# Optimization experiments

Hardware: AMD Instinct MI355X
Metric: run time of the kernel (lower is better)

The kernel has to match this reference:

```python
import jax, jax.numpy as jnp
import numpy as np

B, T, N = 16, 12, 1024
DIM_IN, DOUT, CHEB_K, EMB = 1, 64, 2, 10
TOD, DOW = 48, 7
DIN = DIM_IN + 2 * EMB  # 21: input feature + tod emb + dow emb


def _mk(key, shape, scale=0.1):
    return scale * jax.random.normal(key, shape, dtype=jnp.float32)


def setup_inputs() -> dict:
    key = jax.random.key(0)
    ks = jax.random.split(key, 16)
    data = jax.random.normal(ks[0], (B, T, N, DIM_IN), jnp.float32)
    tod = jax.random.randint(ks[1], (B, T, N), 0, TOD).astype(jnp.float32)
    dow = jax.random.randint(ks[2], (B, T, N), 0, DOW).astype(jnp.float32)
    x = jnp.concatenate([data, tod[..., None], dow[..., None]], axis=-1)
    return dict(
        x=x,
        init_state=jnp.zeros((1, B, N, DOUT), jnp.float32),
        ne_tod=jax.random.normal(ks[3], (B, T, EMB), jnp.float32),
        ne_dow=jax.random.normal(ks[4], (B, T, EMB), jnp.float32),
        node_emb=jax.random.normal(ks[5], (N, EMB), jnp.float32),
        Wtod=_mk(ks[6], (TOD, EMB)), btod=jnp.zeros((EMB,), jnp.float32),
        Wdow=_mk(ks[7], (DOW, EMB)), bdow=jnp.zeros((EMB,), jnp.float32),
        WQ=_mk(ks[8], (DOUT, DOUT)), bQ=jnp.zeros((DOUT,), jnp.float32),
        WK=_mk(ks[9], (DOUT, DOUT)), bK=jnp.zeros((DOUT,), jnp.float32),
        WV=_mk(ks[10], (DOUT, DOUT)), bV=jnp.zeros((DOUT,), jnp.float32),
        Wpool_g=_mk(ks[11], (EMB, CHEB_K, DIN + DOUT, 2 * DOUT)),
        bpool_g=_mk(ks[12], (EMB, 2 * DOUT)),
        Wpool_c=_mk(ks[13], (EMB, CHEB_K, DIN + DOUT, DOUT)),
        bpool_c=_mk(ks[14], (EMB, DOUT)),
    )


def _cheb(A, x):
    # Chebyshev basis: T0=x, T1=A@x, Tk=2A T_{k-1}-T_{k-2}. A:[B,N,N], x:[B,N,F] -> [B,K,N,F]
    outs = [x, jnp.einsum('bnm,bmf->bnf', A, x)]
    for _ in range(CHEB_K - 2):
        outs.append(2.0 * jnp.einsum('bnm,bmf->bnf', A, outs[-1]) - outs[-2])
    return jnp.stack(outs[:CHEB_K], axis=1)


def _gconv(A, x, W, b):
    # node-adaptive graph conv: W:[N,K,F,O] (per-node weights from pool), b:[N,O]
    return jnp.einsum('bknf,nkfo->bno', _cheb(A, x), W) + b


def reference(x, init_state, ne_tod, ne_dow, node_emb, Wtod, btod, Wdow, bdow,
              WQ, bQ, WK, bK, WV, bV, Wpool_g, bpool_g, Wpool_c, bpool_c):
    tod = x[..., -2].astype(jnp.int32)
    dow = x[..., -1].astype(jnp.int32)
    # one_hot @ Linear == embedding gather (same math)
    cur = jnp.concatenate([x[..., :DIM_IN], Wtod[tod] + btod, Wdow[dow] + bdow], axis=-1)

    E = node_emb
    # per-node weights/bias from pools (static over time -> hoisted out of scan)
    Wg = jnp.einsum('nd,dkfo->nkfo', E, Wpool_g)
    bg = E @ bpool_g
    Wc = jnp.einsum('nd,dkfo->nkfo', E, Wpool_c)
    bc = E @ bpool_c

    def step(h, inputs):
        x_t, e1, e2 = inputs
        # dynamic adjacency from time-modulated node embeddings
        d1 = E[None] * e1[:, None, :]  # B,N,d
        d2 = E[None] * e2[:, None, :]
        A = jax.nn.softmax(jax.nn.relu(jnp.einsum('bnd,bmd->bnm', d1, d2)), axis=-1)
        zr = jax.nn.sigmoid(_gconv(A, jnp.concatenate([x_t, h], -1), Wg, bg))
        z, r = jnp.split(zr, 2, axis=-1)
        hc = jnp.tanh(_gconv(A, jnp.concatenate([x_t, z * h], -1), Wc, bc))
        h_new = r * h + (1.0 - r) * hc
        return h_new, h_new

    xs = (jnp.moveaxis(cur, 1, 0), jnp.moveaxis(ne_tod, 1, 0), jnp.moveaxis(ne_dow, 1, 0))
    h_last, states = jax.lax.scan(step, init_state[0], xs)
    seq = jnp.moveaxis(states, 0, 1)  # B,T,N,DOUT

    # temporal self-attention (per node, over T)
    xr = jnp.swapaxes(seq, 1, 2)  # B,N,T,DOUT
    Q = xr @ WQ + bQ
    K = xr @ WK + bK
    V = xr @ WV + bV
    attn = jax.nn.softmax(jnp.einsum('bntd,bnsd->bnts', Q, K) / (DOUT ** 0.5), axis=-1)
    Z = jnp.einsum('bnts,bnsd->bntd', attn, V)
    out = jnp.swapaxes(Z, 1, 2)  # B,T,N,DOUT
    return out, h_last
```

## Files before the change

kernel.cpp:

```cpp
#include <hip/hip_runtime.h>

#define BB 16
#define TT 12
#define NN 1024
#define EMB 10
#define DIN 21
#define DOUT 64
#define FF 85
#define FP 96
#define KFP 176
#define BTN (BB * TT * NN)
#define ASCALE 256.0f
#define INV_ASCALE (1.0f / 256.0f)
#define LSCALE 4096.0f
#define INV_LSCALE (1.0f / 4096.0f)

typedef float4 f4;
typedef _Float16 f16;
typedef __attribute__((ext_vector_type(8))) _Float16 f16x8;
typedef __attribute__((ext_vector_type(4))) float f32x4;

__global__ __launch_bounds__(256) void k_embedT(const float* __restrict__ x,
    const float* __restrict__ Wtod, const float* __restrict__ btod,
    const float* __restrict__ Wdow, const float* __restrict__ bdow,
    f16* __restrict__ curh, f16* __restrict__ curl) {
  int idx = blockIdx.x * 256 + threadIdx.x;
  if (idx >= BB * TT * DIN * NN) return;
  int n = idx & 1023;
  int f = (idx >> 10) % DIN;
  int bt = idx / (DIN * 1024);
  const float* xp = x + ((size_t)bt * 1024 + n) * 3;
  float v;
  if (f == 0) v = xp[0];
  else if (f < 1 + EMB) {
    int tod = (int)xp[1];
    v = Wtod[tod * EMB + f - 1] + btod[f - 1];
  } else {
    int dow = (int)xp[2];
    v = Wdow[dow * EMB + f - 1 - EMB] + bdow[f - 1 - EMB];
  }
  f16 hi = (f16)v;
  curh[idx] = hi;
  curl[idx] = (f16)((v - (float)hi) * LSCALE);
}

__global__ __launch_bounds__(256) void k_wpT(const float* __restrict__ Wpool,
    float* __restrict__ Wp2, int O, int total) {
  int idx = blockIdx.x * 256 + threadIdx.x;
  if (idx >= total) return;
  int j = idx & 7;
  int d = (idx >> 3) % EMB;
  int kc = (idx / (8 * EMB)) % 22;
  int o = idx / (8 * EMB * 22);
  int kf = kc * 8 + j;
  Wp2[idx] = (kf < 2 * FF) ? Wpool[((size_t)d * 2 * FF + kf) * O + o] : 0.f;
}

__global__ __launch_bounds__(256) void k_poolT(const float* __restrict__ E,
    const float* __restrict__ Wp2, f16* __restrict__ Wh, f16* __restrict__ Wl,
    int O, int CH) {
  int n0 = blockIdx.y * 16;
  int c = blockIdx.x * 256 + threadIdx.x;
  __shared__ float Es[16][EMB];
  if (threadIdx.x < 16 * EMB)
    Es[threadIdx.x / EMB][threadIdx.x % EMB] =
        E[(n0 + threadIdx.x / EMB) * EMB + threadIdx.x % EMB];
  __syncthreads();
  if (c >= CH) return;
  const float* wb = Wp2 + (size_t)c * 80;
  float wv[80];
#pragma unroll
  for (int i = 0; i < 20; i++) *(f4*)&wv[i * 4] = *(const f4*)(wb + i * 4);
  for (int ni = 0; ni < 16; ni++) {
    f16x8 hv, lv;
#pragma unroll
    for (int j = 0; j < 8; j++) {
      float v = 0.f;
#pragma unroll
      for (int d = 0; d < EMB; d++) v = fmaf(Es[ni][d], wv[d * 8 + j], v);
      f16 hi = (f16)v;
      hv[j] = hi;
      lv[j] = (f16)((v - (float)hi) * LSCALE);
    }
    size_t base = ((size_t)(n0 + ni) * O * 22 + c) * 8;
    *(f16x8*)(Wh + base) = hv;
    *(f16x8*)(Wl + base) = lv;
  }
}

__global__ __launch_bounds__(256) void k_poolb(const float* __restrict__ E,
    const float* __restrict__ bpool, float* __restrict__ bvec, int O) {
  int idx = blockIdx.x * 256 + threadIdx.x;
  if (idx >= NN * O) return;
  int o = idx % O, n = idx / O;
  float a = 0.f;
#pragma unroll
  for (int d = 0; d < EMB; d++) a += E[n * EMB + d] * bpool[d * O + o];
  bvec[idx] = a;
}

__global__ __launch_bounds__(256) void k_inith(const float* __restrict__ s,
    float* __restrict__ hb, f16* __restrict__ hTh, f16* __restrict__ hTl) {
  int i = blockIdx.x * 256 + threadIdx.x;
  if (i >= BB * NN * DOUT) return;
  float v = s[i];
  hb[i] = v;
  int b = i >> 16;
  int n = (i >> 6) & 1023;
  int o = i & 63;
  f16 hi = (f16)v;
  size_t ti = (((size_t)(b * 64 + o)) << 10) + n;
  hTh[ti] = hi;
  hTl[ti] = (f16)((v - (float)hi) * LSCALE);
}

__global__ __launch_bounds__(256) void k_cvtw(const float* __restrict__ WQ,
    const float* __restrict__ WK, const float* __restrict__ WV,
    const float* __restrict__ bQ, const float* __restrict__ bK, const float* __restrict__ bV,
    f16* __restrict__ wbt, float* __restrict__ biasb) {
  int idx = blockIdx.x * 256 + threadIdx.x;
  if (idx < 3 * DOUT * DOUT) {
    int mat = idx >> 12;
    int d = (idx >> 6) & 63;
    int k = idx & 63;
    const float* W = mat == 0 ? WQ : (mat == 1 ? WK : WV);
    wbt[idx] = (f16)(W[k * DOUT + d]);
  } else if (idx < 3 * DOUT * DOUT + 192) {
    int j = idx - 3 * DOUT * DOUT;
    const float* bb = (j >> 6) == 0 ? bQ : ((j >> 6) == 1 ? bK : bV);
    biasb[j] = bb[j & 63];
  }
}

__global__ __launch_bounds__(256) void k_scores(const float* __restrict__ E,
    const float* __restrict__ ne1, const float* __restrict__ ne2, int t,
    f16* __restrict__ Ah, f16* __restrict__ Al,
    float* __restrict__ T1g, float* __restrict__ T1c) {
  int b = blockIdx.y;
  int i0 = blockIdx.x * 4;
  int tid = threadIdx.x;
  int lane = tid & 63;
  int wid = tid >> 6;
  {
    int gid = (blockIdx.y * gridDim.x + blockIdx.x) * 256 + tid;
    for (int i = gid; i < BB * NN * FP; i += 1048576) T1g[i] = 0.f;
    T1c[gid] = 0.f;
  }
  __shared__ float redm[4][4];
  __shared__ float reds[4][4];
  float g[EMB];
#pragma unroll
  for (int d = 0; d < EMB; d++)
    g[d] = ne1[(b * TT + t) * EMB + d] * ne2[(b * TT + t) * EMB + d];
  float c[4][EMB];
#pragma unroll
  for (int ii = 0; ii < 4; ii++)
#pragma unroll
    for (int d = 0; d < EMB; d++)
      c[ii][d] = E[(i0 + ii) * EMB + d] * g[d];
  float s[4][4];
#pragma unroll
  for (int jj = 0; jj < 4; jj++) {
    int j = jj * 256 + tid;
    float Ej[EMB];
#pragma unroll
    for (int d = 0; d < EMB; d++) Ej[d] = E[j * EMB + d];
#pragma unroll
    for (int ii = 0; ii < 4; ii++) {
      float acc = 0.f;
#pragma unroll
      for (int d = 0; d < EMB; d++) acc = fmaf(c[ii][d], Ej[d], acc);
      s[ii][jj] = fmaxf(acc, 0.f);
    }
  }
  float m4[4];
#pragma unroll
  for (int ii = 0; ii < 4; ii++) {
    float v = fmaxf(fmaxf(s[ii][0], s[ii][1]), fmaxf(s[ii][2], s[ii][3]));
#pragma unroll
    for (int off = 32; off > 0; off >>= 1) v = fmaxf(v, __shfl_xor(v, off));
    if (lane == 0) redm[wid][ii] = v;
  }
  __syncthreads();
#pragma unroll
  for (int ii = 0; ii < 4; ii++)
    m4[ii] = fmaxf(fmaxf(redm[0][ii], redm[1][ii]), fmaxf(redm[2][ii], redm[3][ii]));
  float e[4][4];
  float inv[4];
#pragma unroll
  for (int ii = 0; ii < 4; ii++) {
    float lsum = 0.f;
#pragma unroll
    for (int jj = 0; jj < 4; jj++) { e[ii][jj] = __expf(s[ii][jj] - m4[ii]); lsum += e[ii][jj]; }
#pragma unroll
    for (int off = 32; off > 0; off >>= 1) lsum += __shfl_xor(lsum, off);
    if (lane == 0) reds[wid][ii] = lsum;
  }
  __syncthreads();
#pragma unroll
  for (int ii = 0; ii < 4; ii++)
    inv[ii] = ASCALE / (reds[0][ii] + reds[1][ii] + reds[2][ii] + reds[3][ii]);
#pragma unroll
  for (int ii = 0; ii < 4; ii++) {
    size_t base = ((size_t)(b * NN) + i0 + ii) * NN;
#pragma unroll
    for (int jj = 0; jj < 4; jj++) {
      float a = e[ii][jj] * inv[ii];
      f16 hi = (f16)a;
      Ah[base + jj * 256 + tid] = hi;
      Al[base + jj * 256 + tid] = (f16)((a - (float)hi) * LSCALE);
    }
  }
}

__global__ __launch_bounds__(256) void k_spmv_g(
    const f16* __restrict__ Ah, const f16* __restrict__ Al,
    const f16* __restrict__ curh, const f16* __restrict__ curl, int t,
    const f16* __restrict__ hTh, const f16* __restrict__ hTl,
    float* __restrict__ Y) {
  int b = blockIdx.y;
  int i0 = blockIdx.x * 32;
  int kh = blockIdx.z;
  int tid = threadIdx.x;
  int lane = tid & 63, w = tid >> 6;
  int rg = w & 1, cg = w >> 1;
  int quad = lane >> 4, m = lane & 15;
  __shared__ __align__(16) f16 As_h[32][72];
  __shared__ __align__(16) f16 As_l[32][72];
  __shared__ __align__(16) f16 Xh[96][72];
  __shared__ __align__(16) f16 Xl[96][72];
  for (int q = tid; q < 11 * 72; q += 256) {
    int f = 85 + q / 72, j = q % 72;
    Xh[f][j] = (f16)0.f;
    Xl[f][j] = (f16)0.f;
  }
  f32x4 accH[3], accL[3];
#pragma unroll
  for (int q = 0; q < 3; q++) {
    accH[q] = (f32x4){0.f, 0.f, 0.f, 0.f};
    accL[q] = (f32x4){0.f, 0.f, 0.f, 0.f};
  }
  const f16* Ahb = Ah + ((size_t)(b * NN + i0)) * NN;
  const f16* Alb = Al + ((size_t)(b * NN + i0)) * NN;
  const f16* curhb = curh + ((size_t)(b * TT + t) * DIN) * NN;
  const f16* curlb = curl + ((size_t)(b * TT + t) * DIN) * NN;
  const f16* hThb = hTh + ((size_t)b << 16);
  const f16* hTlb = hTl + ((size_t)b << 16);
  int ar = tid >> 3, ac = (tid & 7) << 3;
  for (int j0 = kh * 512; j0 < kh * 512 + 512; j0 += 64) {
    *(int4*)&As_h[ar][ac] = *(const int4*)(Ahb + (size_t)ar * NN + j0 + ac);
    *(int4*)&As_l[ar][ac] = *(const int4*)(Alb + (size_t)ar * NN + j0 + ac);
#pragma unroll
    for (int p = 0; p < 6; p++) {
      int ch = p * 256 + tid;
      int isl = ch >= 768 ? 1 : 0;
      int idx = ch - isl * 768;
      int row = idx >> 3, cc = (idx & 7) << 3;
      if (row < 85) {
        const f16* s = row < 21
            ? ((isl ? curlb : curhb) + ((size_t)row << 10) + j0 + cc)
            : ((isl ? hTlb : hThb) + ((size_t)(row - 21) << 10) + j0 + cc);
        f16* d = (isl ? &Xl[0][0] : &Xh[0][0]) + row * 72 + cc;
        *(int4*)d = *(const int4*)s;
      }
    }
    __syncthreads();
#pragma unroll
    for (int ks = 0; ks < 2; ks++) {
      int k0 = ks * 32 + quad * 8;
      f16x8 a_h = *(const f16x8*)&As_h[rg * 16 + m][k0];
      f16x8 a_l = *(const f16x8*)&As_l[rg * 16 + m][k0];
#pragma unroll
      for (int nfi = 0; nfi < 3; nfi++) {
        int nf = cg * 3 + nfi;
        f16x8 x_h = *(const f16x8*)&Xh[nf * 16 + m][k0];
        f16x8 x_l = *(const f16x8*)&Xl[nf * 16 + m][k0];
        accH[nfi] = __builtin_amdgcn_mfma_f32_16x16x32_f16(a_h, x_h, accH[nfi], 0, 0, 0);
        accL[nfi] = __builtin_amdgcn_mfma_f32_16x16x32_f16(a_h, x_l, accL[nfi], 0, 0, 0);
        accL[nfi] = __builtin_amdgcn_mfma_f32_16x16x32_f16(a_l, x_h, accL[nfi], 0, 0, 0);
      }
    }
    __syncthreads();
  }
#pragma unroll
  for (int nfi = 0; nfi < 3; nfi++) {
    int nf = cg * 3 + nfi;
#pragma unroll
    for (int reg = 0; reg < 4; reg++) {
      int row = i0 + rg * 16 + quad * 4 + reg;
      atomicAdd(&Y[((size_t)(b * NN) + row) * FP + nf * 16 + m],
                (accH[nfi][reg] + accL[nfi][reg] * INV_LSCALE) * INV_ASCALE);
    }
  }
}

__global__ __launch_bounds__(256) void k_spmv_c(
    const f16* __restrict__ Ah, const f16* __restrict__ Al,
    const f16* __restrict__ zhTh, const f16* __restrict__ zhTl,
    float* __restrict__ Y) {
  int b = blockIdx.y;
  int i0 = blockIdx.x * 32;
  int kh = blockIdx.z;
  int tid = threadIdx.x;
  int lane = tid & 63, w = tid >> 6;
  int rg = w & 1, cg = w >> 1;
  int quad = lane >> 4, m = lane & 15;
  __shared__ __align__(16) f16 As_h[32][72];
  __shared__ __align__(16) f16 As_l[32][72];
  __shared__ __align__(16) f16 Xh[64][72];
  __shared__ __align__(16) f16 Xl[64][72];
  f32x4 accH[2], accL[2];
#pragma unroll
  for (int q = 0; q < 2; q++) {
    accH[q] = (f32x4){0.f, 0.f, 0.f, 0.f};
    accL[q] = (f32x4){0.f, 0.f, 0.f, 0.f};
  }
  const f16* Ahb = Ah + ((size_t)(b * NN + i0)) * NN;
  const f16* Alb = Al + ((size_t)(b * NN + i0)) * NN;
  const f16* zThb = zhTh + ((size_t)b << 16);
  const f16* zTlb = zhTl + ((size_t)b << 16);
  int ar = tid >> 3, ac = (tid & 7) << 3;
  for (int j0 = kh * 512; j0 < kh * 512 + 512; j0 += 64) {
    *(int4*)&As_h[ar][ac] = *(const int4*)(Ahb + (size_t)ar * NN + j0 + ac);
    *(int4*)&As_l[ar][ac] = *(const int4*)(Alb + (size_t)ar * NN + j0 + ac);
#pragma unroll
    for (int p = 0; p < 4; p++) {
      int ch = p * 256 + tid;
      int isl = ch >= 512 ? 1 : 0;
      int idx = ch - isl * 512;
      int row = idx >> 3, cc = (idx & 7) << 3;
      const f16* s = (isl ? zTlb : zThb) + ((size_t)row << 10) + j0 + cc;
      f16* d = (isl ? &Xl[0][0] : &Xh[0][0]) + row * 72 + cc;
      *(int4*)d = *(const int4*)s;
    }
    __syncthreads();
#pragma unroll
    for (int ks = 0; ks < 2; ks++) {
      int k0 = ks * 32 + quad * 8;
      f16x8 a_h = *(const f16x8*)&As_h[rg * 16 + m][k0];
      f16x8 a_l = *(const f16x8*)&As_l[rg * 16 + m][k0];
#pragma unroll
      for (int nfi = 0; nfi < 2; nfi++) {
        int nf = cg * 2 + nfi;
        f16x8 x_h = *(const f16x8*)&Xh[nf * 16 + m][k0];
        f16x8 x_l = *(const f16x8*)&Xl[nf * 16 + m][k0];
        accH[nfi] = __builtin_amdgcn_mfma_f32_16x16x32_f16(a_h, x_h, accH[nfi], 0, 0, 0);
        accL[nfi] = __builtin_amdgcn_mfma_f32_16x16x32_f16(a_h, x_l, accL[nfi], 0, 0, 0);
        accL[nfi] = __builtin_amdgcn_mfma_f32_16x16x32_f16(a_l, x_h, accL[nfi], 0, 0, 0);
      }
    }
    __syncthreads();
  }
#pragma unroll
  for (int nfi = 0; nfi < 2; nfi++) {
    int nf = cg * 2 + nfi;
#pragma unroll
    for (int reg = 0; reg < 4; reg++) {
      int row = i0 + rg * 16 + quad * 4 + reg;
      atomicAdd(&Y[(((size_t)(b * NN) + row) << 6) + nf * 16 + m],
                (accH[nfi][reg] + accL[nfi][reg] * INV_LSCALE) * INV_ASCALE);
    }
  }
}

__global__ __launch_bounds__(256) void k_nodemm_g(
    const f16* __restrict__ curh, const f16* __restrict__ curl, int t,
    const float* __restrict__ hb, const float* __restrict__ T1,
    const f16* __restrict__ Wh, const f16* __restrict__ Wl,
    const float* __restrict__ bg,
    float* __restrict__ r, float* __restrict__ zhb,
    f16* __restrict__ zhTh, f16* __restrict__ zhTl) {
  int n = blockIdx.x, oc = blockIdx.y;
  int tid = threadIdx.x;
  int lane = tid & 63, w = tid >> 6;
  int quad = lane >> 4, m = lane & 15;
  __shared__ __align__(16) f16 Xh[16][200];
  __shared__ __align__(16) f16 Xl[16][200];
  for (int q = tid; q < 16 * 200; q += 256) {
    int bi = q / 200, kf = q % 200;
    f16 hi, lo;
    if (kf < DIN) {
      size_t ci = (((size_t)(bi * TT + t) * DIN) + kf) * NN + n;
      hi = curh[ci];
      lo = curl[ci];
    } else if (kf < 2 * FF) {
      float v = (kf < FF) ? hb[(((size_t)bi << 10) + n) * DOUT + kf - DIN]
                          : T1[(((size_t)bi << 10) + n) * FP + kf - FF];
      hi = (f16)v;
      lo = (f16)((v - (float)hi) * LSCALE);
    } else {
      hi = (f16)0.f;
      lo = (f16)0.f;
    }
    Xh[bi][kf] = hi;
    Xl[bi][kf] = lo;
  }
  __syncthreads();
  f32x4 accH = (f32x4){0.f, 0.f, 0.f, 0.f};
  f32x4 accL = (f32x4){0.f, 0.f, 0.f, 0.f};
  const f16* WhB = Wh + ((size_t)(n * 128 + oc * 64 + w * 16 + m)) * KFP + quad * 8;
  const f16* WlB = Wl + ((size_t)(n * 128 + oc * 64 + w * 16 + m)) * KFP + quad * 8;
#pragma unroll
  for (int ks = 0; ks < 6; ks++) {
    f16x8 b_h = *(const f16x8*)(WhB + ks * 32);
    f16x8 b_l = *(const f16x8*)(WlB + ks * 32);
    int k0 = ks * 32 + quad * 8;
    f16x8 a_h = *(const f16x8*)&Xh[m][k0];
    f16x8 a_l = *(const f16x8*)&Xl[m][k0];
    accH = __builtin_amdgcn_mfma_f32_16x16x32_f16(a_h, b_h, accH, 0, 0, 0);
    accL = __builtin_amdgcn_mfma_f32_16x16x32_f16(a_h, b_l, accL, 0, 0, 0);
    accL = __builtin_amdgcn_mfma_f32_16x16x32_f16(a_l, b_h, accL, 0, 0, 0);
  }
  int o = oc * 64 + w * 16 + m;
  float bias = bg[n * 128 + o];
  if (oc == 0) {
#pragma unroll
    for (int reg = 0; reg < 4; reg++) {
      int bi = quad * 4 + reg;
      float v = accH[reg] + accL[reg] * INV_LSCALE + bias;
      v = 1.f / (1.f + __expf(-v));
      size_t off = (((size_t)bi << 10) + n) * DOUT;
      float zh = v * hb[off + o];
      zhb[off + o] = zh;
      f16 hi = (f16)zh;
      size_t ti = (((size_t)(bi * 64 + o)) << 10) + n;
      zhTh[ti] = hi;
      zhTl[ti] = (f16)((zh - (float)hi) * LSCALE);
    }
  } else {
#pragma unroll
    for (int reg = 0; reg < 4; reg++) {
      int bi = quad * 4 + reg;
      float v = accH[reg] + accL[reg] * INV_LSCALE + bias;
      v = 1.f / (1.f + __expf(-v));
      r[(((size_t)bi << 10) + n) * DOUT + o - DOUT] = v;
    }
  }
}

__global__ __launch_bounds__(256) void k_nodemm_c(
    const f16* __restrict__ curh, const f16* __restrict__ curl, int t,
    const float* __restrict__ hb_in, const float* __restrict__ zhb,
    const float* __restrict__ T1g, const float* __restrict__ T1c,
    const f16* __restrict__ Wh, const f16* __restrict__ Wl,
    const float* __restrict__ bc,
    const float* __restrict__ r, float* __restrict__ hb, f16* __restrict__ seqb,
    f16* __restrict__ hTh, f16* __restrict__ hTl) {
  int n = blockIdx.x;
  int tid = threadIdx.x;
  int lane = tid & 63, w = tid >> 6;
  int quad = lane >> 4, m = lane & 15;
  __shared__ __align__(16) f16 Xh[16][200];
  __shared__ __align__(16) f16 Xl[16][200];
  for (int q = tid; q < 16 * 200; q += 256) {
    int bi = q / 200, kf = q % 200;
    f16 hi, lo;
    if (kf < DIN) {
      size_t ci = (((size_t)(bi * TT + t) * DIN) + kf) * NN + n;
      hi = curh[ci];
      lo = curl[ci];
    } else if (kf < 2 * FF) {
      float v;
      if (kf < FF) v = zhb[(((size_t)bi << 10) + n) * DOUT + kf - DIN];
      else {
        int u = kf - FF;
        v = (u < DIN) ? T1g[(((size_t)bi << 10) + n) * FP + u]
                      : T1c[((((size_t)bi << 10) + n) << 6) + (u - DIN)];
      }
      hi = (f16)v;
      lo = (f16)((v - (float)hi) * LSCALE);
    } else {
      hi = (f16)0.f;
      lo = (f16)0.f;
    }
    Xh[bi][kf] = hi;
    Xl[bi][kf] = lo;
  }
  __syncthreads();
  f32x4 accH = (f32x4){0.f, 0.f, 0.f, 0.f};
  f32x4 accL = (f32x4){0.f, 0.f, 0.f, 0.f};
  const f16* WhB = Wh + ((size_t)(n * 64 + w * 16 + m)) * KFP + quad * 8;
  const f16* WlB = Wl + ((size_t)(n * 64 + w * 16 + m)) * KFP + quad * 8;
#pragma unroll
  for (int ks = 0; ks < 6; ks++) {
    f16x8 b_h = *(const f16x8*)(WhB + ks * 32);
    f16x8 b_l = *(const f16x8*)(WlB + ks * 32);
    int k0 = ks * 32 + quad * 8;
    f16x8 a_h = *(const f16x8*)&Xh[m][k0];
    f16x8 a_l = *(const f16x8*)&Xl[m][k0];
    accH = __builtin_amdgcn_mfma_f32_16x16x32_f16(a_h, b_h, accH, 0, 0, 0);
    accL = __builtin_amdgcn_mfma_f32_16x16x32_f16(a_h, b_l, accL, 0, 0, 0);
    accL = __builtin_amdgcn_mfma_f32_16x16x32_f16(a_l, b_h, accL, 0, 0, 0);
  }
  int o = w * 16 + m;
  float bias = bc[n * 64 + o];
#pragma unroll
  for (int reg = 0; reg < 4; reg++) {
    int bi = quad * 4 + reg;
    float v = accH[reg] + accL[reg] * INV_LSCALE + bias;
    float hc = tanhf(v);
    size_t off = (((size_t)bi << 10) + n) * DOUT + o;
    float rv = r[off];
    float hn = rv * hb_in[off] + (1.f - rv) * hc;
    hb[off] = hn;
    seqb[((size_t)(bi * TT + t) * NN + n) * DOUT + o] = (f16)hn;
    f16 hi = (f16)hn;
    size_t ti = (((size_t)(bi * 64 + o)) << 10) + n;
    hTh[ti] = hi;
    hTl[ti] = (f16)((hn - (float)hi) * LSCALE);
  }
}

__global__ __launch_bounds__(256) void k_qkv(const f16* __restrict__ seqb,
    const f16* __restrict__ wbt, const float* __restrict__ biasb,
    f16* __restrict__ qkvb) {
  int R0 = blockIdx.x * 128;
  int tid = threadIdx.x;
  int lane = tid & 63, w = tid >> 6;
  int quad = lane >> 4, m = lane & 15;
  __shared__ __align__(16) f16 Sb[128][72];
  __shared__ __align__(16) f16 Wt[192][72];
#pragma unroll
  for (int p = 0; p < 4; p++) {
    int q = p * 256 + tid;
    int rr = q >> 3, cc = q & 7;
    *(int4*)&Sb[rr][cc * 8] = *(const int4*)&seqb[((size_t)(R0 + rr) << 6) + cc * 8];
  }
#pragma unroll
  for (int p = 0; p < 6; p++) {
    int q = p * 256 + tid;
    int rr = q >> 3, cc = q & 7;
    *(int4*)&Wt[rr][cc * 8] = *(const int4*)&wbt[((size_t)rr << 6) + cc * 8];
  }
  __syncthreads();
  f32x4 acc[2][12];
#pragma unroll
  for (int mi = 0; mi < 2; mi++)
#pragma unroll
    for (int nf = 0; nf < 12; nf++) acc[mi][nf] = (f32x4){0.f, 0.f, 0.f, 0.f};
#pragma unroll
  for (int ks = 0; ks < 2; ks++) {
    int k0 = ks * 32 + quad * 8;
    f16x8 a0 = *(const f16x8*)&Sb[w * 32 + m][k0];
    f16x8 a1 = *(const f16x8*)&Sb[w * 32 + 16 + m][k0];
#pragma unroll
    for (int nf = 0; nf < 12; nf++) {
      f16x8 bb = *(const f16x8*)&Wt[nf * 16 + m][k0];
      acc[0][nf] = __builtin_amdgcn_mfma_f32_16x16x32_f16(a0, bb, acc[0][nf], 0, 0, 0);
      acc[1][nf] = __builtin_amdgcn_mfma_f32_16x16x32_f16(a1, bb, acc[1][nf], 0, 0, 0);
    }
  }
  float bias_r[12];
#pragma unroll
  for (int nf = 0; nf < 12; nf++) bias_r[nf] = biasb[nf * 16 + m];
#pragma unroll
  for (int mi = 0; mi < 2; mi++) {
#pragma unroll
    for (int nf = 0; nf < 12; nf++) {
      int mat = nf >> 2;
      int d = (nf & 3) * 16 + m;
#pragma unroll
      for (int reg = 0; reg < 4; reg++) {
        int R = R0 + w * 32 + mi * 16 + quad * 4 + reg;
        qkvb[(size_t)mat * BTN * DOUT + ((size_t)R << 6) + d] = (f16)(acc[mi][nf][reg] + bias_r[nf]);
      }
    }
  }
}

__global__ __launch_bounds__(64) void k_attn2(const f16* __restrict__ qkvb,
    float* __restrict__ out) {
  int n = blockIdx.x, b = blockIdx.y;
  int d = threadIdx.x;
  const f16* Qb = qkvb;
  const f16* Kb = qkvb + (size_t)BTN * DOUT;
  const f16* Vb = qkvb + (size_t)2 * BTN * DOUT;
  __shared__ float Qs[TT][65], Ks[TT][65], at[TT][13];
  float vr[TT];
#pragma unroll
  for (int t = 0; t < TT; t++) {
    size_t off = ((size_t)(b * TT + t) * NN + n) * DOUT + d;
    Qs[t][d] = (float)Qb[off];
    Ks[t][d] = (float)Kb[off];
    vr[t] = (float)Vb[off];
  }
  __syncthreads();
  for (int idx = d; idx < TT * TT; idx += 64) {
    int tt = idx / TT, ss = idx % TT;
    float sc = 0.f;
#pragma unroll
    for (int k = 0; k < DOUT; k++) sc = fmaf(Qs[tt][k], Ks[ss][k], sc);
    at[tt][ss] = sc * 0.125f;
  }
  __syncthreads();
  if (d < TT) {
    float mx = -1e30f;
#pragma unroll
    for (int s = 0; s < TT; s++) mx = fmaxf(mx, at[d][s]);
    float sum = 0.f;
#pragma unroll
    for (int s = 0; s < TT; s++) { float e = __expf(at[d][s] - mx); at[d][s] = e; sum += e; }
    float inv = 1.f / sum;
#pragma unroll
    for (int s = 0; s < TT; s++) at[d][s] *= inv;
  }
  __syncthreads();
  float o[TT];
#pragma unroll
  for (int t = 0; t < TT; t++) o[t] = 0.f;
#pragma unroll
  for (int s = 0; s < TT; s++) {
    float vv = vr[s];
#pragma unroll
    for (int t = 0; t < TT; t++) o[t] = fmaf(at[t][s], vv, o[t]);
  }
#pragma unroll
  for (int t = 0; t < TT; t++)
    out[((size_t)(b * TT + t) * NN + n) * DOUT + d] = o[t];
}

__global__ __launch_bounds__(256) void k_hlast(const float* __restrict__ h, float* __restrict__ o) {
  int i = blockIdx.x * 256 + threadIdx.x;
  if (i < BB * NN * DOUT) o[i] = h[i];
}

extern "C" void kernel_launch(void* const* d_in, const int* in_sizes, int n_in,
                              void* d_out, int out_size, void* d_ws, size_t ws_size,
                              hipStream_t stream) {
  const float* x        = (const float*)d_in[0];
  const float* init_st  = (const float*)d_in[1];
  const float* ne_tod   = (const float*)d_in[2];
  const float* ne_dow   = (const float*)d_in[3];
  const float* E        = (const float*)d_in[4];
  const float* Wtod     = (const float*)d_in[5];
  const float* btod     = (const float*)d_in[6];
  const float* Wdow     = (const float*)d_in[7];
  const float* bdow     = (const float*)d_in[8];
  const float* WQ       = (const float*)d_in[9];
  const float* bQ       = (const float*)d_in[10];
  const float* WK       = (const float*)d_in[11];
  const float* bK       = (const float*)d_in[12];
  const float* WV       = (const float*)d_in[13];
  const float* bV       = (const float*)d_in[14];
  const float* Wpool_g  = (const float*)d_in[15];
  const float* bpool_g  = (const float*)d_in[16];
  const float* Wpool_c  = (const float*)d_in[17];
  const float* bpool_c  = (const float*)d_in[18];

  float* out = (float*)d_out;
  float* hlast_out = out + (size_t)BTN * DOUT;
  f16* seqb = (f16*)d_out;

  char* P = (char*)d_ws;
  auto alloc = [&](size_t bytes) { char* r = P; P += (bytes + 255) & ~(size_t)255; return r; };
  f16* curh  = (f16*)alloc((size_t)BB * TT * DIN * NN * 2);
  f16* curl  = (f16*)alloc((size_t)BB * TT * DIN * NN * 2);
  f16* Wgh   = (f16*)alloc((size_t)NN * 128 * KFP * 2);
  f16* Wgl   = (f16*)alloc((size_t)NN * 128 * KFP * 2);
  f16* Wch   = (f16*)alloc((size_t)NN * 64 * KFP * 2);
  f16* Wcl   = (f16*)alloc((size_t)NN * 64 * KFP * 2);
  float* Wp2g = (float*)alloc((size_t)128 * 22 * EMB * 8 * 4);
  float* Wp2c = (float*)alloc((size_t)64 * 22 * EMB * 8 * 4);
  float* bg  = (float*)alloc((size_t)NN * 128 * 4);
  float* bc  = (float*)alloc((size_t)NN * 64 * 4);
  float* hb  = (float*)alloc((size_t)BB * NN * DOUT * 4);
  f16* wbt   = (f16*)alloc((size_t)3 * DOUT * DOUT * 2);
  float* biasb = (float*)alloc(192 * 4);
  float* rb  = (float*)alloc((size_t)BB * NN * DOUT * 4);
  float* zhb = (float*)alloc((size_t)BB * NN * DOUT * 4);
  f16* hTh   = (f16*)alloc((size_t)BB * DOUT * NN * 2);
  f16* hTl   = (f16*)alloc((size_t)BB * DOUT * NN * 2);
  f16* zhTh  = (f16*)alloc((size_t)BB * DOUT * NN * 2);
  f16* zhTl  = (f16*)alloc((size_t)BB * DOUT * NN * 2);
  char* LOOP = P;
  f16* Ah    = (f16*)alloc((size_t)BB * NN * NN * 2);
  f16* Al    = (f16*)alloc((size_t)BB * NN * NN * 2);
  float* T1g = (float*)alloc((size_t)BB * NN * FP * 4);
  float* T1c = (float*)alloc((size_t)BB * NN * DOUT * 4);
  f16* qkvb  = (f16*)LOOP;

  k_embedT<<<(BB * TT * DIN * NN + 255) / 256, 256, 0, stream>>>(x, Wtod, btod, Wdow, bdow, curh, curl);
  {
    int totg = 128 * 22 * EMB * 8;
    int totc = 64 * 22 * EMB * 8;
    k_wpT<<<(totg + 255) / 256, 256, 0, stream>>>(Wpool_g, Wp2g, 128, totg);
    k_wpT<<<(totc + 255) / 256, 256, 0, stream>>>(Wpool_c, Wp2c, 64, totc);
  }
  k_poolT<<<dim3(11, 64), 256, 0, stream>>>(E, Wp2g, Wgh, Wgl, 128, 128 * 22);
  k_poolT<<<dim3(6, 64), 256, 0, stream>>>(E, Wp2c, Wch, Wcl, 64, 64 * 22);
  k_poolb<<<(NN * 128 + 255) / 256, 256, 0, stream>>>(E, bpool_g, bg, 128);
  k_poolb<<<(NN * 64 + 255) / 256, 256, 0, stream>>>(E, bpool_c, bc, 64);
  k_inith<<<(BB * NN * DOUT + 255) / 256, 256, 0, stream>>>(init_st, hb, hTh, hTl);
  k_cvtw<<<(3 * DOUT * DOUT + 192 + 255) / 256, 256, 0, stream>>>(WQ, WK, WV, bQ, bK, bV, wbt, biasb);

  for (int t = 0; t < TT; t++) {
    k_scores<<<dim3(NN / 4, BB), 256, 0, stream>>>(E, ne_tod, ne_dow, t, Ah, Al, T1g, T1c);
    k_spmv_g<<<dim3(NN / 32, BB, 2), 256, 0, stream>>>(Ah, Al, curh, curl, t, hTh, hTl, T1g);
    k_nodemm_g<<<dim3(NN, 2), 256, 0, stream>>>(curh, curl, t, hb, T1g, Wgh, Wgl, bg, rb, zhb, zhTh, zhTl);
    k_spmv_c<<<dim3(NN / 32, BB, 2), 256, 0, stream>>>(Ah, Al, zhTh, zhTl, T1c);
    k_nodemm_c<<<NN, 256, 0, stream>>>(curh, curl, t, hb, zhb, T1g, T1c, Wch, Wcl, bc, rb, hb, seqb, hTh, hTl);
  }

  k_qkv<<<BTN / 128, 256, 0, stream>>>(seqb, wbt, biasb, qkvb);
  k_attn2<<<dim3(NN, BB), 64, 0, stream>>>(qkvb, out);
  k_hlast<<<(BB * NN * DOUT + 255) / 256, 256, 0, stream>>>(hb, hlast_out);
}
```

Baseline: 1.998 ms.

## Recompute softmax adjacency on the fly in spmv kernels instead of materializing it

The scores kernel now stores only each row's softmax max and scaled inverse sum, and no longer writes the full hi/lo fp16 adjacency matrices. Both graph-conv kernels rebuild each 32x64 adjacency tile in shared memory from the node embeddings (via a transposed embedding copy), the per-time gate vector and those row statistics before running the MFMA products. This removes writing and twice reading 2x32MB of adjacency per timestep. In exchange it adds exp and FMA work plus an extra barrier inside each spmv tile loop, and duplicates the recomputation across both kernels.

```diff
diff --git a/kernel.cpp b/kernel.cpp
--- a/kernel.cpp
+++ b/kernel.cpp
@@ -56,6 +56,14 @@
   Wp2[idx] = (kf < 2 * FF) ? Wpool[((size_t)d * 2 * FF + kf) * O + o] : 0.f;
 }
 
+__global__ __launch_bounds__(256) void k_ecolT(const float* __restrict__ E,
+    float* __restrict__ Ecol) {
+  int idx = blockIdx.x * 256 + threadIdx.x;
+  if (idx >= NN * EMB) return;
+  int j = idx / EMB, d = idx % EMB;
+  Ecol[d * NN + j] = E[idx];
+}
+
 __global__ __launch_bounds__(256) void k_poolT(const float* __restrict__ E,
     const float* __restrict__ Wp2, f16* __restrict__ Wh, f16* __restrict__ Wl,
     int O, int CH) {
@@ -134,7 +142,7 @@
 
 __global__ __launch_bounds__(256) void k_scores(const float* __restrict__ E,
     const float* __restrict__ ne1, const float* __restrict__ ne2, int t,
-    f16* __restrict__ Ah, f16* __restrict__ Al,
+    float* __restrict__ Am, float* __restrict__ Ainv,
     float* __restrict__ T1g, float* __restrict__ T1c) {
   int b = blockIdx.y;
   int i0 = blockIdx.x * 4;
@@ -185,13 +193,12 @@
 #pragma unroll
   for (int ii = 0; ii < 4; ii++)
     m4[ii] = fmaxf(fmaxf(redm[0][ii], redm[1][ii]), fmaxf(redm[2][ii], redm[3][ii]));
-  float e[4][4];
   float inv[4];
 #pragma unroll
   for (int ii = 0; ii < 4; ii++) {
     float lsum = 0.f;
 #pragma unroll
-    for (int jj = 0; jj < 4; jj++) { e[ii][jj] = __expf(s[ii][jj] - m4[ii]); lsum += e[ii][jj]; }
+    for (int jj = 0; jj < 4; jj++) lsum += __expf(s[ii][jj] - m4[ii]);
 #pragma unroll
     for (int off = 32; off > 0; off >>= 1) lsum += __shfl_xor(lsum, off);
     if (lane == 0) reds[wid][ii] = lsum;
@@ -200,21 +207,19 @@
 #pragma unroll
   for (int ii = 0; ii < 4; ii++)
     inv[ii] = ASCALE / (reds[0][ii] + reds[1][ii] + reds[2][ii] + reds[3][ii]);
-#pragma unroll
-  for (int ii = 0; ii < 4; ii++) {
-    size_t base = ((size_t)(b * NN) + i0 + ii) * NN;
-#pragma unroll
-    for (int jj = 0; jj < 4; jj++) {
-      float a = e[ii][jj] * inv[ii];
-      f16 hi = (f16)a;
-      Ah[base + jj * 256 + tid] = hi;
-      Al[base + jj * 256 + tid] = (f16)((a - (float)hi) * LSCALE);
+  if (tid == 0) {
+#pragma unroll
+    for (int ii = 0; ii < 4; ii++) {
+      Am[b * NN + i0 + ii] = m4[ii];
+      Ainv[b * NN + i0 + ii] = inv[ii];
     }
   }
 }
 
 __global__ __launch_bounds__(256) void k_spmv_g(
-    const f16* __restrict__ Ah, const f16* __restrict__ Al,
+    const float* __restrict__ E, const float* __restrict__ Ecol,
+    const float* __restrict__ Am, const float* __restrict__ Ainv,
+    const float* __restrict__ ne1, const float* __restrict__ ne2,
     const f16* __restrict__ curh, const f16* __restrict__ curl, int t,
     const f16* __restrict__ hTh, const f16* __restrict__ hTl,
     float* __restrict__ Y) {
@@ -229,6 +234,7 @@
   __shared__ __align__(16) f16 As_l[32][72];
   __shared__ __align__(16) f16 Xh[96][72];
   __shared__ __align__(16) f16 Xl[96][72];
+  __shared__ __align__(16) float Es[EMB][72];
   for (int q = tid; q < 11 * 72; q += 256) {
     int f = 85 + q / 72, j = q % 72;
     Xh[f][j] = (f16)0.f;
@@ -240,16 +246,26 @@
     accH[q] = (f32x4){0.f, 0.f, 0.f, 0.f};
     accL[q] = (f32x4){0.f, 0.f, 0.f, 0.f};
   }
-  const f16* Ahb = Ah + ((size_t)(b * NN + i0)) * NN;
-  const f16* Alb = Al + ((size_t)(b * NN + i0)) * NN;
+  int irow = tid >> 3;
+  int jb = (tid & 7) << 3;
+  float gv[EMB], ci[EMB];
+#pragma unroll
+  for (int d = 0; d < EMB; d++)
+    gv[d] = ne1[(b * TT + t) * EMB + d] * ne2[(b * TT + t) * EMB + d];
+#pragma unroll
+  for (int d = 0; d < EMB; d++)
+    ci[d] = E[(i0 + irow) * EMB + d] * gv[d];
+  float m_i = Am[b * NN + i0 + irow];
+  float inv_i = Ainv[b * NN + i0 + irow];
   const f16* curhb = curh + ((size_t)(b * TT + t) * DIN) * NN;
   const f16* curlb = curl + ((size_t)(b * TT + t) * DIN) * NN;
   const f16* hThb = hTh + ((size_t)b << 16);
   const f16* hTlb = hTl + ((size_t)b << 16);
-  int ar = tid >> 3, ac = (tid & 7) << 3;
   for (int j0 = kh * 512; j0 < kh * 512 + 512; j0 += 64) {
-    *(int4*)&As_h[ar][ac] = *(const int4*)(Ahb + (size_t)ar * NN + j0 + ac);
-    *(int4*)&As_l[ar][ac] = *(const int4*)(Alb + (size_t)ar * NN + j0 + ac);
+    if (tid < 160) {
+      int d = tid / 16, jj = tid % 16;
+      *(f4*)&Es[d][jj * 4] = *(const f4*)&Ecol[d * NN + j0 + jj * 4];
+    }
 #pragma unroll
     for (int p = 0; p < 6; p++) {
       int ch = p * 256 + tid;
@@ -265,6 +281,32 @@
       }
     }
     __syncthreads();
+    {
+      float a8[8];
+#pragma unroll
+      for (int jj = 0; jj < 8; jj++) a8[jj] = 0.f;
+#pragma unroll
+      for (int d = 0; d < EMB; d++) {
+        f4 e0 = *(f4*)&Es[d][jb];
+        f4 e1 = *(f4*)&Es[d][jb + 4];
+        a8[0] = fmaf(ci[d], e0.x, a8[0]); a8[1] = fmaf(ci[d], e0.y, a8[1]);
+        a8[2] = fmaf(ci[d], e0.z, a8[2]); a8[3] = fmaf(ci[d], e0.w, a8[3]);
+        a8[4] = fmaf(ci[d], e1.x, a8[4]); a8[5] = fmaf(ci[d], e1.y, a8[5]);
+        a8[6] = fmaf(ci[d], e1.z, a8[6]); a8[7] = fmaf(ci[d], e1.w, a8[7]);
+      }
+      f16x8 hv, lv;
+#pragma unroll
+      for (int jj = 0; jj < 8; jj++) {
+        float s = fmaxf(a8[jj], 0.f);
+        float a = __expf(s - m_i) * inv_i;
+        f16 hi = (f16)a;
+        hv[jj] = hi;
+        lv[jj] = (f16)((a - (float)hi) * LSCALE);
+      }
+      *(f16x8*)&As_h[irow][jb] = hv;
+      *(f16x8*)&As_l[irow][jb] = lv;
+    }
+    __syncthreads();
 #pragma unroll
     for (int ks = 0; ks < 2; ks++) {
       int k0 = ks * 32 + quad * 8;
@@ -295,7 +337,9 @@
 }
 
 __global__ __launch_bounds__(256) void k_spmv_c(
-    const f16* __restrict__ Ah, const f16* __restrict__ Al,
+    const float* __restrict__ E, const float* __restrict__ Ecol,
+    const float* __restrict__ Am, const float* __restrict__ Ainv,
+    const float* __restrict__ ne1, const float* __restrict__ ne2, int t,
     const f16* __restrict__ zhTh, const f16* __restrict__ zhTl,
     float* __restrict__ Y) {
   int b = blockIdx.y;
@@ -309,20 +353,31 @@
   __shared__ __align__(16) f16 As_l[32][72];
   __shared__ __align__(16) f16 Xh[64][72];
   __shared__ __align__(16) f16 Xl[64][72];
+  __shared__ __align__(16) float Es[EMB][72];
   f32x4 accH[2], accL[2];
 #pragma unroll
   for (int q = 0; q < 2; q++) {
     accH[q] = (f32x4){0.f, 0.f, 0.f, 0.f};
     accL[q] = (f32x4){0.f, 0.f, 0.f, 0.f};
   }
-  const f16* Ahb = Ah + ((size_t)(b * NN + i0)) * NN;
-  const f16* Alb = Al + ((size_t)(b * NN + i0)) * NN;
+  int irow = tid >> 3;
+  int jb = (tid & 7) << 3;
+  float gv[EMB], ci[EMB];
+#pragma unroll
+  for (int d = 0; d < EMB; d++)
+    gv[d] = ne1[(b * TT + t) * EMB + d] * ne2[(b * TT + t) * EMB + d];
+#pragma unroll
+  for (int d = 0; d < EMB; d++)
+    ci[d] = E[(i0 + irow) * EMB + d] * gv[d];
+  float m_i = Am[b * NN + i0 + irow];
+  float inv_i = Ainv[b * NN + i0 + irow];
   const f16* zThb = zhTh + ((size_t)b << 16);
   const f16* zTlb = zhTl + ((size_t)b << 16);
-  int ar = tid >> 3, ac = (tid & 7) << 3;
   for (int j0 = kh * 512; j0 < kh * 512 + 512; j0 += 64) {
-    *(int4*)&As_h[ar][ac] = *(const int4*)(Ahb + (size_t)ar * NN + j0 + ac);
-    *(int4*)&As_l[ar][ac] = *(const int4*)(Alb + (size_t)ar * NN + j0 + ac);
+    if (tid < 160) {
+      int d = tid / 16, jj = tid % 16;
+      *(f4*)&Es[d][jj * 4] = *(const f4*)&Ecol[d * NN + j0 + jj * 4];
+    }
 #pragma unroll
     for (int p = 0; p < 4; p++) {
       int ch = p * 256 + tid;
@@ -332,6 +387,32 @@
       const f16* s = (isl ? zTlb : zThb) + ((size_t)row << 10) + j0 + cc;
       f16* d = (isl ? &Xl[0][0] : &Xh[0][0]) + row * 72 + cc;
       *(int4*)d = *(const int4*)s;
+    }
+    __syncthreads();
+    {
+      float a8[8];
+#pragma unroll
+      for (int jj = 0; jj < 8; jj++) a8[jj] = 0.f;
+#pragma unroll
+      for (int d = 0; d < EMB; d++) {
+        f4 e0 = *(f4*)&Es[d][jb];
+        f4 e1 = *(f4*)&Es[d][jb + 4];
+        a8[0] = fmaf(ci[d], e0.x, a8[0]); a8[1] = fmaf(ci[d], e0.y, a8[1]);
+        a8[2] = fmaf(ci[d], e0.z, a8[2]); a8[3] = fmaf(ci[d], e0.w, a8[3]);
+        a8[4] = fmaf(ci[d], e1.x, a8[4]); a8[5] = fmaf(ci[d], e1.y, a8[5]);
+        a8[6] = fmaf(ci[d], e1.z, a8[6]); a8[7] = fmaf(ci[d], e1.w, a8[7]);
+      }
+      f16x8 hv, lv;
+#pragma unroll
+      for (int jj = 0; jj < 8; jj++) {
+        float s = fmaxf(a8[jj], 0.f);
+        float a = __expf(s - m_i) * inv_i;
+        f16 hi = (f16)a;
+        hv[jj] = hi;
+        lv[jj] = (f16)((a - (float)hi) * LSCALE);
+      }
+      *(f16x8*)&As_h[irow][jb] = hv;
+      *(f16x8*)&As_l[irow][jb] = lv;
     }
     __syncthreads();
 #pragma unroll
@@ -673,10 +754,11 @@
   f16* zhTh  = (f16*)alloc((size_t)BB * DOUT * NN * 2);
   f16* zhTl  = (f16*)alloc((size_t)BB * DOUT * NN * 2);
   char* LOOP = P;
-  f16* Ah    = (f16*)alloc((size_t)BB * NN * NN * 2);
-  f16* Al    = (f16*)alloc((size_t)BB * NN * NN * 2);
   float* T1g = (float*)alloc((size_t)BB * NN * FP * 4);
   float* T1c = (float*)alloc((size_t)BB * NN * DOUT * 4);
+  float* Am  = (float*)alloc((size_t)BB * NN * 4);
+  float* Ainv= (float*)alloc((size_t)BB * NN * 4);
+  float* Ecol= (float*)alloc((size_t)EMB * NN * 4);
   f16* qkvb  = (f16*)LOOP;
 
   k_embedT<<<(BB * TT * DIN * NN + 255) / 256, 256, 0, stream>>>(x, Wtod, btod, Wdow, bdow, curh, curl);
@@ -686,6 +768,7 @@
     k_wpT<<<(totg + 255) / 256, 256, 0, stream>>>(Wpool_g, Wp2g, 128, totg);
     k_wpT<<<(totc + 255) / 256, 256, 0, stream>>>(Wpool_c, Wp2c, 64, totc);
   }
+  k_ecolT<<<(NN * EMB + 255) / 256, 256, 0, stream>>>(E, Ecol);
   k_poolT<<<dim3(11, 64), 256, 0, stream>>>(E, Wp2g, Wgh, Wgl, 128, 128 * 22);
   k_poolT<<<dim3(6, 64), 256, 0, stream>>>(E, Wp2c, Wch, Wcl, 64, 64 * 22);
   k_poolb<<<(NN * 128 + 255) / 256, 256, 0, stream>>>(E, bpool_g, bg, 128);
@@ -694,10 +777,10 @@
   k_cvtw<<<(3 * DOUT * DOUT + 192 + 255) / 256, 256, 0, stream>>>(WQ, WK, WV, bQ, bK, bV, wbt, biasb);
 
   for (int t = 0; t < TT; t++) {
-    k_scores<<<dim3(NN / 4, BB), 256, 0, stream>>>(E, ne_tod, ne_dow, t, Ah, Al, T1g, T1c);
-    k_spmv_g<<<dim3(NN / 32, BB, 2), 256, 0, stream>>>(Ah, Al, curh, curl, t, hTh, hTl, T1g);
+    k_scores<<<dim3(NN / 4, BB), 256, 0, stream>>>(E, ne_tod, ne_dow, t, Am, Ainv, T1g, T1c);
+    k_spmv_g<<<dim3(NN / 32, BB, 2), 256, 0, stream>>>(E, Ecol, Am, Ainv, ne_tod, ne_dow, curh, curl, t, hTh, hTl, T1g);
     k_nodemm_g<<<dim3(NN, 2), 256, 0, stream>>>(curh, curl, t, hb, T1g, Wgh, Wgl, bg, rb, zhb, zhTh, zhTl);
-    k_spmv_c<<<dim3(NN / 32, BB, 2), 256, 0, stream>>>(Ah, Al, zhTh, zhTl, T1c);
+    k_spmv_c<<<dim3(NN / 32, BB, 2), 256, 0, stream>>>(E, Ecol, Am, Ainv, ne_tod, ne_dow, t, zhTh, zhTl, T1c);
     k_nodemm_c<<<NN, 256, 0, stream>>>(curh, curl, t, hb, zhb, T1g, T1c, Wch, Wcl, bc, rb, hb, seqb, hTh, hTl);
   }
 
```

Result: slower. 2.058 ms (+3.0%).
